# Kernel optimization log

Hardware: AMD Instinct MI355X
Metric: run time of the kernel (lower is better)

## Reference

```python
import jax, jax.numpy as jnp
import numpy as np

N = 100000   # nodes
E = 220000   # directed edges (each branch)
H = 128      # hidden_dim
OUT = 1      # output_dim
G = 4096     # num graphs in batch
PE = 5       # laplacian eigenvector PE dims
VOCAB = 28   # atom types


def gcn_conv(x, src, dst, W, b, n):
    # PyG GCNConv: x' = D^-1/2 (A + I) D^-1/2 (X W) + b
    h = x @ W
    deg = jax.ops.segment_sum(jnp.ones(src.shape[0], x.dtype), dst, num_segments=n) + 1.0
    dinv = jax.lax.rsqrt(deg)
    coef = dinv[src] * dinv[dst]                                    # [E]
    agg = jax.ops.segment_sum(h[src] * coef[:, None], dst, num_segments=n)
    agg = agg + h * (dinv * dinv)[:, None]                          # self-loop term
    return agg + b


def gcn2(x, edge_index, W1, b1, W2, b2, n):
    # PyG GCN model, num_layers=2: conv -> relu -> conv
    src, dst = edge_index[0], edge_index[1]
    h = jax.nn.relu(gcn_conv(x, src, dst, W1, b1, n))
    return gcn_conv(h, src, dst, W2, b2, n)


def setup_inputs() -> dict:
    key = jax.random.key(0)
    ks = jax.random.split(key, 16)
    s = 0.1
    return {
        "node_tokens": jax.random.randint(ks[0], (N, 1), 0, VOCAB),
        "pe": jax.random.normal(ks[1], (N, PE), jnp.float32),
        "edge_index": jax.random.randint(ks[2], (2, E), 0, N),
        "vr_edge_index": jax.random.randint(ks[3], (2, E), 0, N),
        "batch": jnp.sort(jax.random.randint(ks[4], (N,), 0, G)),
        "embed_table": jax.random.normal(ks[5], (VOCAB, H), jnp.float32) * s,
        "Wt": jax.random.normal(ks[6], (PE, H), jnp.float32) * s,
        "bt": jnp.zeros((H,), jnp.float32),
        "W1": jax.random.normal(ks[7], (H, H), jnp.float32) * s,
        "b1": jnp.zeros((H,), jnp.float32),
        "W2": jax.random.normal(ks[8], (H, OUT), jnp.float32) * s,
        "b2": jnp.zeros((OUT,), jnp.float32),
        "Wv1": jax.random.normal(ks[9], (H, H), jnp.float32) * s,
        "bv1": jnp.zeros((H,), jnp.float32),
        "Wv2": jax.random.normal(ks[10], (H, OUT), jnp.float32) * s,
        "bv2": jnp.zeros((OUT,), jnp.float32),
    }


def reference(node_tokens, pe, edge_index, vr_edge_index, batch, embed_table,
              Wt, bt, W1, b1, W2, b2, Wv1, bv1, Wv2, bv2):
    # embed_x(data.x.long()).squeeze(1) + lin_trans(pe)
    x = embed_table[node_tokens[:, 0]] + (pe @ Wt + bt)             # [N, H]
    x1 = gcn2(x, edge_index, W1, b1, W2, b2, N)                     # [N, OUT]
    xv = gcn2(x, vr_edge_index, Wv1, bv1, Wv2, bv2, N)              # [N, OUT]
    x1 = x1 + xv
    y_hat = jax.ops.segment_sum(x1, batch, num_segments=G)          # [G, OUT]
    y_hat = jnp.squeeze(y_hat, axis=-1)                             # [G]
    return (y_hat, x)
```

## Files before the change

### kernel.cpp

```cpp
#include <hip/hip_runtime.h>

#define NN 100000
#define NE 220000
#define HD 128
#define NG 4096
#define NPE 5
#define NB_SCAN ((NN + 255) / 256)
#define NBX4 ((NN * HD / 4) / 256)
#define NBW 128
#define NBD ((2 * NE + 255) / 256)

typedef unsigned int uint;
typedef unsigned short ushort;
typedef __attribute__((ext_vector_type(8))) short bf16x8;
typedef __attribute__((ext_vector_type(4))) float f32x4;

__device__ __forceinline__ float bf2f(uint u16) {
    return __uint_as_float(u16 << 16);
}
__device__ __forceinline__ ushort f2bf(float f) {
    uint u = __float_as_uint(f);
    u += 0x7fffu + ((u >> 16) & 1u);
    return (ushort)(u >> 16);
}

__global__ void k_front(const int* __restrict__ tok, const float* __restrict__ pe,
                        const float* __restrict__ embed, const float* __restrict__ Wtr,
                        const float* __restrict__ bt,
                        float* __restrict__ x, ushort* __restrict__ xb,
                        const float* __restrict__ W1, const float* __restrict__ Wv1,
                        ushort* __restrict__ Wcat,
                        const int* __restrict__ ei, const int* __restrict__ vei,
                        int* __restrict__ cnt) {
    int b = blockIdx.x;
    if (b < NBX4) {
        int idx = b * 256 + threadIdx.x;
        int n = idx >> 5, q = idx & 31;
        int t = tok[n];
        float4 acc = ((const float4*)(embed + (size_t)t * HD))[q];
        float4 bv = ((const float4*)bt)[q];
        acc.x += bv.x; acc.y += bv.y; acc.z += bv.z; acc.w += bv.w;
        const float* pen = pe + n * NPE;
#pragma unroll
        for (int k = 0; k < NPE; ++k) {
            float p = pen[k];
            float4 wv = ((const float4*)(Wtr + k * HD))[q];
            acc.x += p * wv.x; acc.y += p * wv.y;
            acc.z += p * wv.z; acc.w += p * wv.w;
        }
        ((float4*)x)[idx] = acc;
        uint2 pk;
        pk.x = (uint)f2bf(acc.x) | ((uint)f2bf(acc.y) << 16);
        pk.y = (uint)f2bf(acc.z) | ((uint)f2bf(acc.w) << 16);
        ((uint2*)xb)[idx] = pk;
    } else if (b < NBX4 + NBW) {
        int t = (b - NBX4) * 256 + threadIdx.x;
        int f = t >> 7, k = t & 127;
        const float* W = (f < HD) ? W1 : Wv1;
        Wcat[t] = f2bf(W[k * HD + (f & 127)]);
    } else {
        int t = (b - NBX4 - NBW) * 256 + threadIdx.x;
        if (t < 2 * NE) {
            int br = t >= NE;
            int e = t - br * NE;
            const int* S = br ? vei : ei;
            atomicAdd(&cnt[br * NN + S[NE + e]], 1);
        }
    }
}

#define LDP 136
__global__ __launch_bounds__(256) void k_gemm(const ushort* __restrict__ xb,
                                              const ushort* __restrict__ Wt,
                                              ushort* __restrict__ H) {
    __shared__ ushort Ws[128 * LDP];
    __shared__ ushort As[128 * LDP];
    int bi = blockIdx.x;
    int fh = bi & 1;
    int n0 = (bi >> 1) * 128;
    int tid = threadIdx.x;
    {
        const uint4* src = (const uint4*)(Wt + (size_t)fh * 128 * 128);
        uint4* dst = (uint4*)Ws;
        for (int i = tid; i < 2048; i += 256) dst[(i >> 4) * 17 + (i & 15)] = src[i];
    }
    {
        uint4* dst = (uint4*)As;
        for (int i = tid; i < 2048; i += 256) {
            int n = n0 + (i >> 4);
            uint4 v = {0u, 0u, 0u, 0u};
            if (n < NN) v = ((const uint4*)(xb + (size_t)n * HD))[i & 15];
            dst[(i >> 4) * 17 + (i & 15)] = v;
        }
    }
    __syncthreads();
    int w = tid >> 6, lane = tid & 63;
    int m = lane & 15, quad = lane >> 4;
    f32x4 acc[2][8] = {};
#pragma unroll
    for (int kc = 0; kc < 4; ++kc) {
        int k0 = kc * 32 + quad * 8;
        bf16x8 xf[2], wf[8];
#pragma unroll
        for (int nt = 0; nt < 2; ++nt)
            xf[nt] = *(const bf16x8*)&As[((w * 2 + nt) * 16 + m) * LDP + k0];
#pragma unroll
        for (int ft = 0; ft < 8; ++ft)
            wf[ft] = *(const bf16x8*)&Ws[(ft * 16 + m) * LDP + k0];
#pragma unroll
        for (int nt = 0; nt < 2; ++nt)
#pragma unroll
            for (int ft = 0; ft < 8; ++ft)
                acc[nt][ft] = __builtin_amdgcn_mfma_f32_16x16x32_bf16(
                    wf[ft], xf[nt], acc[nt][ft], 0, 0, 0);
    }
#pragma unroll
    for (int nt = 0; nt < 2; ++nt) {
        int n = n0 + (w * 2 + nt) * 16 + m;
        if (n >= NN) continue;
#pragma unroll
        for (int ft = 0; ft < 8; ++ft) {
            f32x4 a = acc[nt][ft];
            uint2 pk;
            pk.x = (uint)f2bf(a[0]) | ((uint)f2bf(a[1]) << 16);
            pk.y = (uint)f2bf(a[2]) | ((uint)f2bf(a[3]) << 16);
            *(uint2*)&H[(size_t)n * 256 + fh * 128 + ft * 16 + quad * 4] = pk;
        }
    }
}

__global__ void k_scan1(const int* __restrict__ cnt, int* __restrict__ off,
                        int* __restrict__ bsum, float* __restrict__ dinv) {
    __shared__ int s[256];
    int br = blockIdx.x / NB_SCAN;
    int blk = blockIdx.x % NB_SCAN;
    int tid = threadIdx.x;
    int i = blk * 256 + tid;
    int v = (i < NN) ? cnt[br * NN + i] : 0;
    if (i < NN) dinv[br * NN + i] = rsqrtf((float)v + 1.0f);
    s[tid] = v;
    __syncthreads();
    for (int d = 1; d < 256; d <<= 1) {
        int t = (tid >= d) ? s[tid - d] : 0;
        __syncthreads();
        s[tid] += t;
        __syncthreads();
    }
    if (i < NN) off[br * NN + i] = s[tid] - v;
    if (tid == 255) bsum[br * 512 + blk] = s[255];
}

__global__ void k_scan2(int* __restrict__ bsum) {
    __shared__ int s[512];
    int br = blockIdx.x;
    int tid = threadIdx.x;
    int v = (tid < NB_SCAN) ? bsum[br * 512 + tid] : 0;
    s[tid] = v;
    __syncthreads();
    for (int d = 1; d < 512; d <<= 1) {
        int t = (tid >= d) ? s[tid - d] : 0;
        __syncthreads();
        s[tid] += t;
        __syncthreads();
    }
    if (tid < NB_SCAN) bsum[br * 512 + tid] = s[tid] - v;
}

__global__ void k_scan3(int* __restrict__ off, const int* __restrict__ bsum,
                        int* __restrict__ cur) {
    int br = blockIdx.x / NB_SCAN;
    int blk = blockIdx.x % NB_SCAN;
    int i = blk * 256 + threadIdx.x;
    if (i < NN) {
        int o = off[br * NN + i] + bsum[br * 512 + blk];
        off[br * NN + i] = o;
        cur[br * NN + i] = o;
    }
}

__global__ void k_scatter(const int* __restrict__ ei, const int* __restrict__ vei,
                          const float* __restrict__ dinv, int* __restrict__ cur,
                          int2* __restrict__ ent) {
    int t = blockIdx.x * blockDim.x + threadIdx.x;
    if (t >= 2 * NE) return;
    int br = t >= NE;
    int e = t - br * NE;
    const int* S = br ? vei : ei;
    int s = S[e], d = S[NE + e];
    int pos = atomicAdd(&cur[br * NN + d], 1);
    int2 rec;
    rec.x = s;
    rec.y = __float_as_int(dinv[br * NN + s] * dinv[br * NN + d]);
    ent[br * NE + pos] = rec;
}

__global__ void k_gather_ep(const ushort* __restrict__ H, const float* __restrict__ dinv,
                            const int* __restrict__ off, const int* __restrict__ cur,
                            const int2* __restrict__ ent,
                            const float* __restrict__ b1, const float* __restrict__ bv1,
                            const float* __restrict__ W2, const float* __restrict__ Wv2,
                            float* __restrict__ z) {
    int wid = threadIdx.x >> 6;
    int lane = threadIdx.x & 63;
    int half = lane >> 5;
    int l = lane & 31;
    int task = blockIdx.x * 8 + wid * 2 + half;
    int br = task >= NN;
    int n = task - br * NN;

    const int2* en = ent + br * NE;
    size_t hoff = (size_t)br * 128;

    float dv = dinv[br * NN + n];
    uint2 u = *(const uint2*)(H + (size_t)n * 256 + hoff + l * 4);
    float c = dv * dv;
    float a0 = bf2f(u.x & 0xffffu) * c, a1 = bf2f(u.x >> 16) * c;
    float a2 = bf2f(u.y & 0xffffu) * c, a3 = bf2f(u.y >> 16) * c;

    int p0 = off[br * NN + n], p1 = cur[br * NN + n];
    for (int p = p0; p < p1; p += 4) {
        int2 e0 = en[p], e1 = en[p + 1], e2 = en[p + 2], e3 = en[p + 3];
        int s0 = e0.x;
        int s1 = (p + 1 < p1) ? e1.x : n;
        int s2 = (p + 2 < p1) ? e2.x : n;
        int s3 = (p + 3 < p1) ? e3.x : n;
        float c0 = __int_as_float(e0.y);
        float c1 = (p + 1 < p1) ? __int_as_float(e1.y) : 0.f;
        float c2 = (p + 2 < p1) ? __int_as_float(e2.y) : 0.f;
        float c3 = (p + 3 < p1) ? __int_as_float(e3.y) : 0.f;
        uint2 v0 = *(const uint2*)(H + (size_t)s0 * 256 + hoff + l * 4);
        uint2 v1 = *(const uint2*)(H + (size_t)s1 * 256 + hoff + l * 4);
        uint2 v2 = *(const uint2*)(H + (size_t)s2 * 256 + hoff + l * 4);
        uint2 v3 = *(const uint2*)(H + (size_t)s3 * 256 + hoff + l * 4);
        a0 += bf2f(v0.x & 0xffffu) * c0; a1 += bf2f(v0.x >> 16) * c0;
        a2 += bf2f(v0.y & 0xffffu) * c0; a3 += bf2f(v0.y >> 16) * c0;
        a0 += bf2f(v1.x & 0xffffu) * c1; a1 += bf2f(v1.x >> 16) * c1;
        a2 += bf2f(v1.y & 0xffffu) * c1; a3 += bf2f(v1.y >> 16) * c1;
        a0 += bf2f(v2.x & 0xffffu) * c2; a1 += bf2f(v2.x >> 16) * c2;
        a2 += bf2f(v2.y & 0xffffu) * c2; a3 += bf2f(v2.y >> 16) * c2;
        a0 += bf2f(v3.x & 0xffffu) * c3; a1 += bf2f(v3.x >> 16) * c3;
        a2 += bf2f(v3.y & 0xffffu) * c3; a3 += bf2f(v3.y >> 16) * c3;
    }

    const float* bb = br ? bv1 : b1;
    const float* ww = br ? Wv2 : W2;
    float4 b4 = *(const float4*)&bb[l * 4];
    float4 w4 = *(const float4*)&ww[l * 4];
    float part = fmaxf(a0 + b4.x, 0.f) * w4.x + fmaxf(a1 + b4.y, 0.f) * w4.y
               + fmaxf(a2 + b4.z, 0.f) * w4.z + fmaxf(a3 + b4.w, 0.f) * w4.w;
#pragma unroll
    for (int o = 16; o > 0; o >>= 1) part += __shfl_down(part, o, 32);
    if (l == 0) z[br * NN + n] = part;
}

__global__ void k_final2(const float* __restrict__ z, const float* __restrict__ dinv,
                         const int* __restrict__ off, const int* __restrict__ cur,
                         const int2* __restrict__ ent,
                         const float* __restrict__ b2, const float* __restrict__ bv2,
                         const int* __restrict__ batch, float* __restrict__ y) {
    __shared__ float ybuf[256];
    __shared__ int gbase_s;
    int br = blockIdx.x >= NB_SCAN;
    int nb = blockIdx.x - br * NB_SCAN;
    int tid = threadIdx.x;
    ybuf[tid] = 0.f;
    if (tid == 0) gbase_s = batch[nb * 256];
    __syncthreads();
    int gbase = gbase_s;
    int n = nb * 256 + tid;
    if (n < NN) {
        const int2* en = ent + br * NE;
        float dv = dinv[br * NN + n];
        float acc = z[br * NN + n] * dv * dv;
        int p1 = cur[br * NN + n];
        for (int p = off[br * NN + n]; p < p1; p += 4) {
            int2 e0 = en[p], e1 = en[p + 1], e2 = en[p + 2], e3 = en[p + 3];
            int s0 = e0.x;
            int s1 = (p + 1 < p1) ? e1.x : n;
            int s2 = (p + 2 < p1) ? e2.x : n;
            int s3 = (p + 3 < p1) ? e3.x : n;
            float c0 = __int_as_float(e0.y);
            float c1 = (p + 1 < p1) ? __int_as_float(e1.y) : 0.f;
            float c2 = (p + 2 < p1) ? __int_as_float(e2.y) : 0.f;
            float c3 = (p + 3 < p1) ? __int_as_float(e3.y) : 0.f;
            acc += c0 * z[br * NN + s0] + c1 * z[br * NN + s1]
                 + c2 * z[br * NN + s2] + c3 * z[br * NN + s3];
        }
        acc += br ? bv2[0] : b2[0];
        int gi = batch[n] - gbase;
        if (gi < 256) atomicAdd(&ybuf[gi], acc);
        else atomicAdd(&y[batch[n]], acc);
    }
    __syncthreads();
    float v = ybuf[tid];
    if (v != 0.f) atomicAdd(&y[gbase + tid], v);
}

extern "C" void kernel_launch(void* const* d_in, const int* in_sizes, int n_in,
                              void* d_out, int out_size, void* d_ws, size_t ws_size,
                              hipStream_t stream) {
    const int*   tok   = (const int*)d_in[0];
    const float* pe    = (const float*)d_in[1];
    const int*   ei    = (const int*)d_in[2];
    const int*   vei   = (const int*)d_in[3];
    const int*   batch = (const int*)d_in[4];
    const float* embed = (const float*)d_in[5];
    const float* Wtr   = (const float*)d_in[6];
    const float* bt    = (const float*)d_in[7];
    const float* W1    = (const float*)d_in[8];
    const float* b1    = (const float*)d_in[9];
    const float* W2    = (const float*)d_in[10];
    const float* b2    = (const float*)d_in[11];
    const float* Wv1   = (const float*)d_in[12];
    const float* bv1   = (const float*)d_in[13];
    const float* Wv2   = (const float*)d_in[14];
    const float* bv2   = (const float*)d_in[15];

    float* y = (float*)d_out;
    float* x = y + NG;

    char* w = (char*)d_ws;
    ushort* xb   = (ushort*)w;               w += (size_t)NN * HD * 2;
    ushort* H    = (ushort*)w;               w += (size_t)NN * 256 * 2;
    ushort* Wcat = (ushort*)w;               w += 256 * 128 * 2;
    float*  dinv = (float*)w;                w += 2 * NN * 4;
    float*  z    = (float*)w;                w += 2 * NN * 4;
    int*    cnt  = (int*)w;                  w += 2 * NN * 4;
    int*    off  = (int*)w;                  w += 2 * NN * 4;
    int*    cur  = (int*)w;                  w += 2 * NN * 4;
    int2*   ent  = (int2*)w;                 w += (size_t)(2 * NE + 8) * 8;
    int*    bsum = (int*)w;                  w += 2 * 512 * 4;

    hipMemsetAsync(y, 0, NG * sizeof(float), stream);
    hipMemsetAsync(cnt, 0, 2 * NN * sizeof(int), stream);

    k_front<<<NBX4 + NBW + NBD, 256, 0, stream>>>(tok, pe, embed, Wtr, bt, x, xb,
                                                  W1, Wv1, Wcat, ei, vei, cnt);
    k_gemm<<<2 * ((NN + 127) / 128), 256, 0, stream>>>(xb, Wcat, H);
    k_scan1<<<2 * NB_SCAN, 256, 0, stream>>>(cnt, off, bsum, dinv);
    k_scan2<<<2, 512, 0, stream>>>(bsum);
    k_scan3<<<2 * NB_SCAN, 256, 0, stream>>>(off, bsum, cur);
    k_scatter<<<(2 * NE + 255) / 256, 256, 0, stream>>>(ei, vei, dinv, cur, ent);
    k_gather_ep<<<2 * NN / 8, 256, 0, stream>>>(H, dinv, off, cur, ent,
                                                b1, bv1, W2, Wv2, z);
    k_final2<<<2 * NB_SCAN, 256, 0, stream>>>(z, dinv, off, cur, ent,
                                              b2, bv2, batch, y);
}
```

Measured before the change: 243.5 us.

## Aggregate before GEMM and fuse layer-1 aggregation, GEMM and epilogue

Uses linearity (A·X)·W = A·(X·W) to aggregate the 128-dim bf16 input features over neighbours first, stage the result in shared memory, then run the MFMA GEMM and the ReLU·W2 epilogue in the same kernel. This drops the separate GEMM kernel and the 51 MB intermediate H buffer, and gathers from the 25.6 MB xb instead of a strided half of H. In exchange, W fragments are read straight from global memory instead of shared memory. The aggregated result is also rounded to bf16 before the GEMM, which adds a rounding step.

```diff
diff --git a/kernel.cpp b/kernel.cpp
--- a/kernel.cpp
+++ b/kernel.cpp
@@ -9,6 +9,8 @@
 #define NBX4 ((NN * HD / 4) / 256)
 #define NBW 128
 #define NBD ((2 * NE + 255) / 256)
+#define NBAG ((NN + 63) / 64)
+#define LDP 136
 
 typedef unsigned int uint;
 typedef unsigned short ushort;
@@ -69,66 +71,6 @@
     }
 }
 
-#define LDP 136
-__global__ __launch_bounds__(256) void k_gemm(const ushort* __restrict__ xb,
-                                              const ushort* __restrict__ Wt,
-                                              ushort* __restrict__ H) {
-    __shared__ ushort Ws[128 * LDP];
-    __shared__ ushort As[128 * LDP];
-    int bi = blockIdx.x;
-    int fh = bi & 1;
-    int n0 = (bi >> 1) * 128;
-    int tid = threadIdx.x;
-    {
-        const uint4* src = (const uint4*)(Wt + (size_t)fh * 128 * 128);
-        uint4* dst = (uint4*)Ws;
-        for (int i = tid; i < 2048; i += 256) dst[(i >> 4) * 17 + (i & 15)] = src[i];
-    }
-    {
-        uint4* dst = (uint4*)As;
-        for (int i = tid; i < 2048; i += 256) {
-            int n = n0 + (i >> 4);
-            uint4 v = {0u, 0u, 0u, 0u};
-            if (n < NN) v = ((const uint4*)(xb + (size_t)n * HD))[i & 15];
-            dst[(i >> 4) * 17 + (i & 15)] = v;
-        }
-    }
-    __syncthreads();
-    int w = tid >> 6, lane = tid & 63;
-    int m = lane & 15, quad = lane >> 4;
-    f32x4 acc[2][8] = {};
-#pragma unroll
-    for (int kc = 0; kc < 4; ++kc) {
-        int k0 = kc * 32 + quad * 8;
-        bf16x8 xf[2], wf[8];
-#pragma unroll
-        for (int nt = 0; nt < 2; ++nt)
-            xf[nt] = *(const bf16x8*)&As[((w * 2 + nt) * 16 + m) * LDP + k0];
-#pragma unroll
-        for (int ft = 0; ft < 8; ++ft)
-            wf[ft] = *(const bf16x8*)&Ws[(ft * 16 + m) * LDP + k0];
-#pragma unroll
-        for (int nt = 0; nt < 2; ++nt)
-#pragma unroll
-            for (int ft = 0; ft < 8; ++ft)
-                acc[nt][ft] = __builtin_amdgcn_mfma_f32_16x16x32_bf16(
-                    wf[ft], xf[nt], acc[nt][ft], 0, 0, 0);
-    }
-#pragma unroll
-    for (int nt = 0; nt < 2; ++nt) {
-        int n = n0 + (w * 2 + nt) * 16 + m;
-        if (n >= NN) continue;
-#pragma unroll
-        for (int ft = 0; ft < 8; ++ft) {
-            f32x4 a = acc[nt][ft];
-            uint2 pk;
-            pk.x = (uint)f2bf(a[0]) | ((uint)f2bf(a[1]) << 16);
-            pk.y = (uint)f2bf(a[2]) | ((uint)f2bf(a[3]) << 16);
-            *(uint2*)&H[(size_t)n * 256 + fh * 128 + ft * 16 + quad * 4] = pk;
-        }
-    }
-}
-
 __global__ void k_scan1(const int* __restrict__ cnt, int* __restrict__ off,
                         int* __restrict__ bsum, float* __restrict__ dinv) {
     __shared__ int s[256];
@@ -194,63 +136,95 @@
     ent[br * NE + pos] = rec;
 }
 
-__global__ void k_gather_ep(const ushort* __restrict__ H, const float* __restrict__ dinv,
-                            const int* __restrict__ off, const int* __restrict__ cur,
-                            const int2* __restrict__ ent,
-                            const float* __restrict__ b1, const float* __restrict__ bv1,
-                            const float* __restrict__ W2, const float* __restrict__ Wv2,
-                            float* __restrict__ z) {
-    int wid = threadIdx.x >> 6;
-    int lane = threadIdx.x & 63;
-    int half = lane >> 5;
-    int l = lane & 31;
-    int task = blockIdx.x * 8 + wid * 2 + half;
-    int br = task >= NN;
-    int n = task - br * NN;
-
-    const int2* en = ent + br * NE;
-    size_t hoff = (size_t)br * 128;
-
-    float dv = dinv[br * NN + n];
-    uint2 u = *(const uint2*)(H + (size_t)n * 256 + hoff + l * 4);
-    float c = dv * dv;
-    float a0 = bf2f(u.x & 0xffffu) * c, a1 = bf2f(u.x >> 16) * c;
-    float a2 = bf2f(u.y & 0xffffu) * c, a3 = bf2f(u.y >> 16) * c;
-
-    int p0 = off[br * NN + n], p1 = cur[br * NN + n];
-    for (int p = p0; p < p1; p += 4) {
-        int2 e0 = en[p], e1 = en[p + 1], e2 = en[p + 2], e3 = en[p + 3];
-        int s0 = e0.x;
-        int s1 = (p + 1 < p1) ? e1.x : n;
-        int s2 = (p + 2 < p1) ? e2.x : n;
-        int s3 = (p + 3 < p1) ? e3.x : n;
-        float c0 = __int_as_float(e0.y);
-        float c1 = (p + 1 < p1) ? __int_as_float(e1.y) : 0.f;
-        float c2 = (p + 2 < p1) ? __int_as_float(e2.y) : 0.f;
-        float c3 = (p + 3 < p1) ? __int_as_float(e3.y) : 0.f;
-        uint2 v0 = *(const uint2*)(H + (size_t)s0 * 256 + hoff + l * 4);
-        uint2 v1 = *(const uint2*)(H + (size_t)s1 * 256 + hoff + l * 4);
-        uint2 v2 = *(const uint2*)(H + (size_t)s2 * 256 + hoff + l * 4);
-        uint2 v3 = *(const uint2*)(H + (size_t)s3 * 256 + hoff + l * 4);
-        a0 += bf2f(v0.x & 0xffffu) * c0; a1 += bf2f(v0.x >> 16) * c0;
-        a2 += bf2f(v0.y & 0xffffu) * c0; a3 += bf2f(v0.y >> 16) * c0;
-        a0 += bf2f(v1.x & 0xffffu) * c1; a1 += bf2f(v1.x >> 16) * c1;
-        a2 += bf2f(v1.y & 0xffffu) * c1; a3 += bf2f(v1.y >> 16) * c1;
-        a0 += bf2f(v2.x & 0xffffu) * c2; a1 += bf2f(v2.x >> 16) * c2;
-        a2 += bf2f(v2.y & 0xffffu) * c2; a3 += bf2f(v2.y >> 16) * c2;
-        a0 += bf2f(v3.x & 0xffffu) * c3; a1 += bf2f(v3.x >> 16) * c3;
-        a2 += bf2f(v3.y & 0xffffu) * c3; a3 += bf2f(v3.y >> 16) * c3;
-    }
-
+__global__ __launch_bounds__(256) void k_agg_gemm(
+        const ushort* __restrict__ xb, const ushort* __restrict__ Wcat,
+        const float* __restrict__ dinv, const int* __restrict__ off,
+        const int* __restrict__ cur, const int2* __restrict__ ent,
+        const float* __restrict__ b1, const float* __restrict__ bv1,
+        const float* __restrict__ W2, const float* __restrict__ Wv2,
+        float* __restrict__ z) {
+    __shared__ ushort As[64 * LDP];
+    int bi = blockIdx.x;
+    int br = bi >= NBAG;
+    int n0 = (bi - br * NBAG) * 64;
+    int tid = threadIdx.x;
+
+    {
+        int hw = tid >> 5;
+        int l = tid & 31;
+        const int2* en = ent + br * NE;
+        for (int nn = 0; nn < 8; ++nn) {
+            int nl = hw * 8 + nn;
+            int n = n0 + nl;
+            uint2 pk = {0u, 0u};
+            if (n < NN) {
+                float dv = dinv[br * NN + n];
+                uint2 u = *(const uint2*)(xb + (size_t)n * HD + l * 4);
+                float c = dv * dv;
+                float a0 = bf2f(u.x & 0xffffu) * c, a1 = bf2f(u.x >> 16) * c;
+                float a2 = bf2f(u.y & 0xffffu) * c, a3 = bf2f(u.y >> 16) * c;
+                int p0 = off[br * NN + n], p1 = cur[br * NN + n];
+                for (int p = p0; p < p1; p += 4) {
+                    int2 e0 = en[p], e1 = en[p + 1], e2 = en[p + 2], e3 = en[p + 3];
+                    int s0 = e0.x;
+                    int s1 = (p + 1 < p1) ? e1.x : n;
+                    int s2 = (p + 2 < p1) ? e2.x : n;
+                    int s3 = (p + 3 < p1) ? e3.x : n;
+                    float c0 = __int_as_float(e0.y);
+                    float c1 = (p + 1 < p1) ? __int_as_float(e1.y) : 0.f;
+                    float c2 = (p + 2 < p1) ? __int_as_float(e2.y) : 0.f;
+                    float c3 = (p + 3 < p1) ? __int_as_float(e3.y) : 0.f;
+                    uint2 v0 = *(const uint2*)(xb + (size_t)s0 * HD + l * 4);
+                    uint2 v1 = *(const uint2*)(xb + (size_t)s1 * HD + l * 4);
+                    uint2 v2 = *(const uint2*)(xb + (size_t)s2 * HD + l * 4);
+                    uint2 v3 = *(const uint2*)(xb + (size_t)s3 * HD + l * 4);
+                    a0 += bf2f(v0.x & 0xffffu) * c0; a1 += bf2f(v0.x >> 16) * c0;
+                    a2 += bf2f(v0.y & 0xffffu) * c0; a3 += bf2f(v0.y >> 16) * c0;
+                    a0 += bf2f(v1.x & 0xffffu) * c1; a1 += bf2f(v1.x >> 16) * c1;
+                    a2 += bf2f(v1.y & 0xffffu) * c1; a3 += bf2f(v1.y >> 16) * c1;
+                    a0 += bf2f(v2.x & 0xffffu) * c2; a1 += bf2f(v2.x >> 16) * c2;
+                    a2 += bf2f(v2.y & 0xffffu) * c2; a3 += bf2f(v2.y >> 16) * c2;
+                    a0 += bf2f(v3.x & 0xffffu) * c3; a1 += bf2f(v3.x >> 16) * c3;
+                    a2 += bf2f(v3.y & 0xffffu) * c3; a3 += bf2f(v3.y >> 16) * c3;
+                }
+                pk.x = (uint)f2bf(a0) | ((uint)f2bf(a1) << 16);
+                pk.y = (uint)f2bf(a2) | ((uint)f2bf(a3) << 16);
+            }
+            *(uint2*)&As[nl * LDP + l * 4] = pk;
+        }
+    }
+    __syncthreads();
+
+    int w = tid >> 6, lane = tid & 63;
+    int m = lane & 15, quad = lane >> 4;
+    const ushort* Wg = Wcat + (size_t)br * 128 * 128;
+    f32x4 acc[8] = {};
+#pragma unroll
+    for (int kc = 0; kc < 4; ++kc) {
+        int k0 = kc * 32 + quad * 8;
+        bf16x8 xf = *(const bf16x8*)&As[(w * 16 + m) * LDP + k0];
+#pragma unroll
+        for (int ft = 0; ft < 8; ++ft) {
+            bf16x8 wf = *(const bf16x8*)&Wg[(ft * 16 + m) * 128 + k0];
+            acc[ft] = __builtin_amdgcn_mfma_f32_16x16x32_bf16(wf, xf, acc[ft], 0, 0, 0);
+        }
+    }
     const float* bb = br ? bv1 : b1;
     const float* ww = br ? Wv2 : W2;
-    float4 b4 = *(const float4*)&bb[l * 4];
-    float4 w4 = *(const float4*)&ww[l * 4];
-    float part = fmaxf(a0 + b4.x, 0.f) * w4.x + fmaxf(a1 + b4.y, 0.f) * w4.y
-               + fmaxf(a2 + b4.z, 0.f) * w4.z + fmaxf(a3 + b4.w, 0.f) * w4.w;
+    float part = 0.f;
 #pragma unroll
-    for (int o = 16; o > 0; o >>= 1) part += __shfl_down(part, o, 32);
-    if (l == 0) z[br * NN + n] = part;
+    for (int ft = 0; ft < 8; ++ft) {
+        int f0 = ft * 16 + quad * 4;
+        float4 b4 = *(const float4*)&bb[f0];
+        float4 w4 = *(const float4*)&ww[f0];
+        f32x4 a = acc[ft];
+        part += fmaxf(a[0] + b4.x, 0.f) * w4.x + fmaxf(a[1] + b4.y, 0.f) * w4.y
+              + fmaxf(a[2] + b4.z, 0.f) * w4.z + fmaxf(a[3] + b4.w, 0.f) * w4.w;
+    }
+    part += __shfl_xor(part, 16);
+    part += __shfl_xor(part, 32);
+    int n = n0 + w * 16 + m;
+    if (quad == 0 && n < NN) z[br * NN + n] = part;
 }
 
 __global__ void k_final2(const float* __restrict__ z, const float* __restrict__ dinv,
@@ -321,7 +295,6 @@
 
     char* w = (char*)d_ws;
     ushort* xb   = (ushort*)w;               w += (size_t)NN * HD * 2;
-    ushort* H    = (ushort*)w;               w += (size_t)NN * 256 * 2;
     ushort* Wcat = (ushort*)w;               w += 256 * 128 * 2;
     float*  dinv = (float*)w;                w += 2 * NN * 4;
     float*  z    = (float*)w;                w += 2 * NN * 4;
@@ -336,13 +309,12 @@
 
     k_front<<<NBX4 + NBW + NBD, 256, 0, stream>>>(tok, pe, embed, Wtr, bt, x, xb,
                                                   W1, Wv1, Wcat, ei, vei, cnt);
-    k_gemm<<<2 * ((NN + 127) / 128), 256, 0, stream>>>(xb, Wcat, H);
     k_scan1<<<2 * NB_SCAN, 256, 0, stream>>>(cnt, off, bsum, dinv);
     k_scan2<<<2, 512, 0, stream>>>(bsum);
     k_scan3<<<2 * NB_SCAN, 256, 0, stream>>>(off, bsum, cur);
     k_scatter<<<(2 * NE + 255) / 256, 256, 0, stream>>>(ei, vei, dinv, cur, ent);
-    k_gather_ep<<<2 * NN / 8, 256, 0, stream>>>(H, dinv, off, cur, ent,
-                                                b1, bv1, W2, Wv2, z);
+    k_agg_gemm<<<2 * NBAG, 256, 0, stream>>>(xb, Wcat, dinv, off, cur, ent,
+                                             b1, bv1, W2, Wv2, z);
     k_final2<<<2 * NB_SCAN, 256, 0, stream>>>(z, dinv, off, cur, ent,
                                               b2, bv2, batch, y);
 }
```

Result: slower. 274.6 us (+12.8%).

## Fuse embedding front-end into GEMM, drop memsets, pack CSR offsets

Applied to the files above, without the earlier changes.

Each GEMM block now computes its 128 embedded rows straight into shared memory and produces both 128-column weight halves, which removes the bf16 xb round trip through global memory and a kernel launch. Weights are read directly from global/L2 instead of being staged in LDS. The two memsets are replaced by zeroing inside a new prep kernel (cnt) and inside k_scan1 (y). Start and end offsets are packed into one int2 array so gather kernels do a single load. Risks: fewer blocks in the fused GEMM, uncached weight fragment loads from global memory, and an extra kernel that must run before the front-end.

```diff
diff --git a/kernel.cpp b/kernel.cpp
--- a/kernel.cpp
+++ b/kernel.cpp
@@ -6,9 +6,11 @@
 #define NG 4096
 #define NPE 5
 #define NB_SCAN ((NN + 255) / 256)
-#define NBX4 ((NN * HD / 4) / 256)
+#define NBF ((NN + 127) / 128)
 #define NBW 128
+#define NBZ ((2 * NN + 255) / 256)
 #define NBD ((2 * NE + 255) / 256)
+#define LDP 136
 
 typedef unsigned int uint;
 typedef unsigned short ushort;
@@ -24,42 +26,96 @@
     return (ushort)(u >> 16);
 }
 
-__global__ void k_front(const int* __restrict__ tok, const float* __restrict__ pe,
-                        const float* __restrict__ embed, const float* __restrict__ Wtr,
-                        const float* __restrict__ bt,
-                        float* __restrict__ x, ushort* __restrict__ xb,
-                        const float* __restrict__ W1, const float* __restrict__ Wv1,
-                        ushort* __restrict__ Wcat,
-                        const int* __restrict__ ei, const int* __restrict__ vei,
-                        int* __restrict__ cnt) {
+__global__ void k_prep0(const float* __restrict__ W1, const float* __restrict__ Wv1,
+                        ushort* __restrict__ Wcat, int* __restrict__ cnt) {
     int b = blockIdx.x;
-    if (b < NBX4) {
-        int idx = b * 256 + threadIdx.x;
-        int n = idx >> 5, q = idx & 31;
-        int t = tok[n];
-        float4 acc = ((const float4*)(embed + (size_t)t * HD))[q];
-        float4 bv = ((const float4*)bt)[q];
-        acc.x += bv.x; acc.y += bv.y; acc.z += bv.z; acc.w += bv.w;
-        const float* pen = pe + n * NPE;
-#pragma unroll
-        for (int k = 0; k < NPE; ++k) {
-            float p = pen[k];
-            float4 wv = ((const float4*)(Wtr + k * HD))[q];
-            acc.x += p * wv.x; acc.y += p * wv.y;
-            acc.z += p * wv.z; acc.w += p * wv.w;
-        }
-        ((float4*)x)[idx] = acc;
-        uint2 pk;
-        pk.x = (uint)f2bf(acc.x) | ((uint)f2bf(acc.y) << 16);
-        pk.y = (uint)f2bf(acc.z) | ((uint)f2bf(acc.w) << 16);
-        ((uint2*)xb)[idx] = pk;
-    } else if (b < NBX4 + NBW) {
-        int t = (b - NBX4) * 256 + threadIdx.x;
+    if (b < NBW) {
+        int t = b * 256 + threadIdx.x;
         int f = t >> 7, k = t & 127;
         const float* W = (f < HD) ? W1 : Wv1;
         Wcat[t] = f2bf(W[k * HD + (f & 127)]);
     } else {
-        int t = (b - NBX4 - NBW) * 256 + threadIdx.x;
+        int t = (b - NBW) * 256 + threadIdx.x;
+        if (t < 2 * NN) cnt[t] = 0;
+    }
+}
+
+__global__ __launch_bounds__(256) void k_front_gemm(
+        const int* __restrict__ tok, const float* __restrict__ pe,
+        const float* __restrict__ embed, const float* __restrict__ Wtr,
+        const float* __restrict__ bt, float* __restrict__ x,
+        const ushort* __restrict__ Wcat, ushort* __restrict__ H,
+        const int* __restrict__ ei, const int* __restrict__ vei,
+        int* __restrict__ cnt) {
+    __shared__ ushort As[128 * LDP];
+    int b = blockIdx.x;
+    if (b < NBF) {
+        int tid = threadIdx.x;
+        int n0 = b * 128;
+        int q = tid & 31;
+        int nlb = tid >> 5;
+        for (int r = 0; r < 16; ++r) {
+            int nl = r * 8 + nlb;
+            int n = n0 + nl;
+            uint2 pk = {0u, 0u};
+            if (n < NN) {
+                int t = tok[n];
+                float4 acc = ((const float4*)(embed + (size_t)t * HD))[q];
+                float4 bv = ((const float4*)bt)[q];
+                acc.x += bv.x; acc.y += bv.y; acc.z += bv.z; acc.w += bv.w;
+                const float* pen = pe + n * NPE;
+#pragma unroll
+                for (int k = 0; k < NPE; ++k) {
+                    float p = pen[k];
+                    float4 wv = ((const float4*)(Wtr + k * HD))[q];
+                    acc.x += p * wv.x; acc.y += p * wv.y;
+                    acc.z += p * wv.z; acc.w += p * wv.w;
+                }
+                ((float4*)x)[n * 32 + q] = acc;
+                pk.x = (uint)f2bf(acc.x) | ((uint)f2bf(acc.y) << 16);
+                pk.y = (uint)f2bf(acc.z) | ((uint)f2bf(acc.w) << 16);
+            }
+            *(uint2*)&As[nl * LDP + q * 4] = pk;
+        }
+        __syncthreads();
+        int w = tid >> 6, lane = tid & 63;
+        int m = lane & 15, quad = lane >> 4;
+#pragma unroll
+        for (int fh = 0; fh < 2; ++fh) {
+            const ushort* Wg = Wcat + (size_t)fh * 128 * 128;
+            f32x4 acc[2][8] = {};
+#pragma unroll
+            for (int kc = 0; kc < 4; ++kc) {
+                int k0 = kc * 32 + quad * 8;
+                bf16x8 xf[2];
+#pragma unroll
+                for (int nt = 0; nt < 2; ++nt)
+                    xf[nt] = *(const bf16x8*)&As[((w * 2 + nt) * 16 + m) * LDP + k0];
+#pragma unroll
+                for (int ft = 0; ft < 8; ++ft) {
+                    bf16x8 wf = *(const bf16x8*)&Wg[(ft * 16 + m) * 128 + k0];
+#pragma unroll
+                    for (int nt = 0; nt < 2; ++nt)
+                        acc[nt][ft] = __builtin_amdgcn_mfma_f32_16x16x32_bf16(
+                            wf, xf[nt], acc[nt][ft], 0, 0, 0);
+                }
+            }
+#pragma unroll
+            for (int nt = 0; nt < 2; ++nt) {
+                int n = n0 + (w * 2 + nt) * 16 + m;
+                if (n >= NN) continue;
+#pragma unroll
+                for (int ft = 0; ft < 8; ++ft) {
+                    f32x4 a = acc[nt][ft];
+                    uint2 pk;
+                    pk.x = (uint)f2bf(a[0]) | ((uint)f2bf(a[1]) << 16);
+                    pk.y = (uint)f2bf(a[2]) | ((uint)f2bf(a[3]) << 16);
+                    *(uint2*)&H[(size_t)n * 256 + fh * 128 + ft * 16 + quad * 4] = pk;
+                }
+            }
+        }
+    } else {
+        int t = (b - NBF) * 256 + threadIdx.x;
         if (t < 2 * NE) {
             int br = t >= NE;
             int e = t - br * NE;
@@ -69,72 +125,15 @@
     }
 }
 
-#define LDP 136
-__global__ __launch_bounds__(256) void k_gemm(const ushort* __restrict__ xb,
-                                              const ushort* __restrict__ Wt,
-                                              ushort* __restrict__ H) {
-    __shared__ ushort Ws[128 * LDP];
-    __shared__ ushort As[128 * LDP];
-    int bi = blockIdx.x;
-    int fh = bi & 1;
-    int n0 = (bi >> 1) * 128;
+__global__ void k_scan1(const int* __restrict__ cnt, int* __restrict__ off,
+                        int* __restrict__ bsum, float* __restrict__ dinv,
+                        float* __restrict__ y) {
+    __shared__ int s[256];
     int tid = threadIdx.x;
-    {
-        const uint4* src = (const uint4*)(Wt + (size_t)fh * 128 * 128);
-        uint4* dst = (uint4*)Ws;
-        for (int i = tid; i < 2048; i += 256) dst[(i >> 4) * 17 + (i & 15)] = src[i];
-    }
-    {
-        uint4* dst = (uint4*)As;
-        for (int i = tid; i < 2048; i += 256) {
-            int n = n0 + (i >> 4);
-            uint4 v = {0u, 0u, 0u, 0u};
-            if (n < NN) v = ((const uint4*)(xb + (size_t)n * HD))[i & 15];
-            dst[(i >> 4) * 17 + (i & 15)] = v;
-        }
-    }
-    __syncthreads();
-    int w = tid >> 6, lane = tid & 63;
-    int m = lane & 15, quad = lane >> 4;
-    f32x4 acc[2][8] = {};
-#pragma unroll
-    for (int kc = 0; kc < 4; ++kc) {
-        int k0 = kc * 32 + quad * 8;
-        bf16x8 xf[2], wf[8];
-#pragma unroll
-        for (int nt = 0; nt < 2; ++nt)
-            xf[nt] = *(const bf16x8*)&As[((w * 2 + nt) * 16 + m) * LDP + k0];
-#pragma unroll
-        for (int ft = 0; ft < 8; ++ft)
-            wf[ft] = *(const bf16x8*)&Ws[(ft * 16 + m) * LDP + k0];
-#pragma unroll
-        for (int nt = 0; nt < 2; ++nt)
-#pragma unroll
-            for (int ft = 0; ft < 8; ++ft)
-                acc[nt][ft] = __builtin_amdgcn_mfma_f32_16x16x32_bf16(
-                    wf[ft], xf[nt], acc[nt][ft], 0, 0, 0);
-    }
-#pragma unroll
-    for (int nt = 0; nt < 2; ++nt) {
-        int n = n0 + (w * 2 + nt) * 16 + m;
-        if (n >= NN) continue;
-#pragma unroll
-        for (int ft = 0; ft < 8; ++ft) {
-            f32x4 a = acc[nt][ft];
-            uint2 pk;
-            pk.x = (uint)f2bf(a[0]) | ((uint)f2bf(a[1]) << 16);
-            pk.y = (uint)f2bf(a[2]) | ((uint)f2bf(a[3]) << 16);
-            *(uint2*)&H[(size_t)n * 256 + fh * 128 + ft * 16 + quad * 4] = pk;
-        }
-    }
-}
-
-__global__ void k_scan1(const int* __restrict__ cnt, int* __restrict__ off,
-                        int* __restrict__ bsum, float* __restrict__ dinv) {
-    __shared__ int s[256];
+    int gid = blockIdx.x * 256 + tid;
+    if (gid < NG) y[gid] = 0.f;
     int br = blockIdx.x / NB_SCAN;
     int blk = blockIdx.x % NB_SCAN;
-    int tid = threadIdx.x;
     int i = blk * 256 + tid;
     int v = (i < NN) ? cnt[br * NN + i] : 0;
     if (i < NN) dinv[br * NN + i] = rsqrtf((float)v + 1.0f);
@@ -166,14 +165,18 @@
     if (tid < NB_SCAN) bsum[br * 512 + tid] = s[tid] - v;
 }
 
-__global__ void k_scan3(int* __restrict__ off, const int* __restrict__ bsum,
+__global__ void k_scan3(const int* __restrict__ off, const int* __restrict__ bsum,
+                        const int* __restrict__ cnt, int2* __restrict__ off2,
                         int* __restrict__ cur) {
     int br = blockIdx.x / NB_SCAN;
     int blk = blockIdx.x % NB_SCAN;
     int i = blk * 256 + threadIdx.x;
     if (i < NN) {
         int o = off[br * NN + i] + bsum[br * 512 + blk];
-        off[br * NN + i] = o;
+        int2 pr;
+        pr.x = o;
+        pr.y = o + cnt[br * NN + i];
+        off2[br * NN + i] = pr;
         cur[br * NN + i] = o;
     }
 }
@@ -195,7 +198,7 @@
 }
 
 __global__ void k_gather_ep(const ushort* __restrict__ H, const float* __restrict__ dinv,
-                            const int* __restrict__ off, const int* __restrict__ cur,
+                            const int2* __restrict__ off2,
                             const int2* __restrict__ ent,
                             const float* __restrict__ b1, const float* __restrict__ bv1,
                             const float* __restrict__ W2, const float* __restrict__ Wv2,
@@ -217,7 +220,8 @@
     float a0 = bf2f(u.x & 0xffffu) * c, a1 = bf2f(u.x >> 16) * c;
     float a2 = bf2f(u.y & 0xffffu) * c, a3 = bf2f(u.y >> 16) * c;
 
-    int p0 = off[br * NN + n], p1 = cur[br * NN + n];
+    int2 pr = off2[br * NN + n];
+    int p0 = pr.x, p1 = pr.y;
     for (int p = p0; p < p1; p += 4) {
         int2 e0 = en[p], e1 = en[p + 1], e2 = en[p + 2], e3 = en[p + 3];
         int s0 = e0.x;
@@ -254,7 +258,7 @@
 }
 
 __global__ void k_final2(const float* __restrict__ z, const float* __restrict__ dinv,
-                         const int* __restrict__ off, const int* __restrict__ cur,
+                         const int2* __restrict__ off2,
                          const int2* __restrict__ ent,
                          const float* __restrict__ b2, const float* __restrict__ bv2,
                          const int* __restrict__ batch, float* __restrict__ y) {
@@ -272,8 +276,9 @@
         const int2* en = ent + br * NE;
         float dv = dinv[br * NN + n];
         float acc = z[br * NN + n] * dv * dv;
-        int p1 = cur[br * NN + n];
-        for (int p = off[br * NN + n]; p < p1; p += 4) {
+        int2 pr = off2[br * NN + n];
+        int p1 = pr.y;
+        for (int p = pr.x; p < p1; p += 4) {
             int2 e0 = en[p], e1 = en[p + 1], e2 = en[p + 2], e3 = en[p + 3];
             int s0 = e0.x;
             int s1 = (p + 1 < p1) ? e1.x : n;
@@ -320,7 +325,6 @@
     float* x = y + NG;
 
     char* w = (char*)d_ws;
-    ushort* xb   = (ushort*)w;               w += (size_t)NN * HD * 2;
     ushort* H    = (ushort*)w;               w += (size_t)NN * 256 * 2;
     ushort* Wcat = (ushort*)w;               w += 256 * 128 * 2;
     float*  dinv = (float*)w;                w += 2 * NN * 4;
@@ -328,21 +332,19 @@
     int*    cnt  = (int*)w;                  w += 2 * NN * 4;
     int*    off  = (int*)w;                  w += 2 * NN * 4;
     int*    cur  = (int*)w;                  w += 2 * NN * 4;
+    int2*   off2 = (int2*)w;                 w += (size_t)2 * NN * 8;
     int2*   ent  = (int2*)w;                 w += (size_t)(2 * NE + 8) * 8;
     int*    bsum = (int*)w;                  w += 2 * 512 * 4;
 
-    hipMemsetAsync(y, 0, NG * sizeof(float), stream);
-    hipMemsetAsync(cnt, 0, 2 * NN * sizeof(int), stream);
-
-    k_front<<<NBX4 + NBW + NBD, 256, 0, stream>>>(tok, pe, embed, Wtr, bt, x, xb,
-                                                  W1, Wv1, Wcat, ei, vei, cnt);
-    k_gemm<<<2 * ((NN + 127) / 128), 256, 0, stream>>>(xb, Wcat, H);
-    k_scan1<<<2 * NB_SCAN, 256, 0, stream>>>(cnt, off, bsum, dinv);
+    k_prep0<<<NBW + NBZ, 256, 0, stream>>>(W1, Wv1, Wcat, cnt);
+    k_front_gemm<<<NBF + NBD, 256, 0, stream>>>(tok, pe, embed, Wtr, bt, x,
+                                                Wcat, H, ei, vei, cnt);
+    k_scan1<<<2 * NB_SCAN, 256, 0, stream>>>(cnt, off, bsum, dinv, y);
     k_scan2<<<2, 512, 0, stream>>>(bsum);
-    k_scan3<<<2 * NB_SCAN, 256, 0, stream>>>(off, bsum, cur);
-    k_scatter<<<(2 * NE + 255) / 256, 256, 0, stream>>>(ei, vei, dinv, cur, ent);
-    k_gather_ep<<<2 * NN / 8, 256, 0, stream>>>(H, dinv, off, cur, ent,
+    k_scan3<<<2 * NB_SCAN, 256, 0, stream>>>(off, bsum, cnt, off2, cur);
+    k_scatter<<<NBD, 256, 0, stream>>>(ei, vei, dinv, cur, ent);
+    k_gather_ep<<<2 * NN / 8, 256, 0, stream>>>(H, dinv, off2, ent,
                                                 b1, bv1, W2, Wv2, z);
-    k_final2<<<2 * NB_SCAN, 256, 0, stream>>>(z, dinv, off, cur, ent,
+    k_final2<<<2 * NB_SCAN, 256, 0, stream>>>(z, dinv, off2, ent,
                                               b2, bv2, batch, y);
 }
```

Result: no change. 243.7 us (+0.1%).
